# Optimization experiments

Measured on AMD Instinct MI355X. Metric: run time of the kernel, lower is better.

The kernel has to match this reference:

```python
import jax, jax.numpy as jnp
import numpy as np

B = 1
FRAMES = 16
P = 64            # patch_dim = image_size // patch_size = 256 // 4
C = 512           # query_dim == hidden_dim
T, HW, WW = 2, 8, 8   # window_size
NH = 8            # num_heads
HD = C // NH      # head_dim = 64
N = FRAMES * P * P


def setup_inputs() -> dict:
    key = jax.random.key(0)
    ks = jax.random.split(key, 5)
    x = jax.random.normal(ks[0], (B, N, C), dtype=jnp.float32)
    Wq = jax.random.normal(ks[1], (C, C), dtype=jnp.float32) * 0.02
    Wk = jax.random.normal(ks[2], (C, C), dtype=jnp.float32) * 0.02
    Wv = jax.random.normal(ks[3], (C, C), dtype=jnp.float32) * 0.02
    Wo = jax.random.normal(ks[4], (C, C), dtype=jnp.float32) * 0.02
    bo = jnp.zeros((C,), dtype=jnp.float32)
    return {"x": x, "Wq": Wq, "Wk": Wk, "Wv": Wv, "Wo": Wo, "bo": bo}


def reference(x, Wq, Wk, Wv, Wo, bo):
    nT, nH, nW = FRAMES // T, P // HW, P // WW
    L = T * HW * WW            # tokens per window = 128
    NWIN = nT * nH * nW        # 512 windows

    # window partition: [B,N,C] -> [B,nWin,L,C]
    xw = x.reshape(B, nT, T, nH, HW, nW, WW, C)
    xw = xw.transpose(0, 1, 3, 5, 2, 4, 6, 7).reshape(B, NWIN, L, C)

    # QKV projections (torch Linear: y = x @ W.T), split heads
    q = (xw @ Wq.T).reshape(B, NWIN, L, NH, HD)
    k = (xw @ Wk.T).reshape(B, NWIN, L, NH, HD)
    v = (xw @ Wv.T).reshape(B, NWIN, L, NH, HD)

    scale = 1.0 / jnp.sqrt(jnp.float32(HD))
    attn = jnp.einsum('bwqhd,bwkhd->bwhqk', q, k) * scale
    attn = jax.nn.softmax(attn, axis=-1)
    out = jnp.einsum('bwhqk,bwkhd->bwqhd', attn, v).reshape(B, NWIN, L, C)

    out = out @ Wo.T + bo      # output projection (dropout is identity at p=0/eval)

    # window merge: inverse of partition
    y = out.reshape(B, nT, nH, nW, T, HW, WW, C)
    y = y.transpose(0, 1, 4, 2, 5, 3, 6, 7).reshape(B, N, C)
    return y
```

## Files before the change

kernel.cpp:

```cpp
#include <hip/hip_runtime.h>


typedef __bf16 bf16x8 __attribute__((ext_vector_type(8)));
typedef float  f32x4  __attribute__((ext_vector_type(4)));

__device__ __forceinline__ unsigned short f2bf(float f) {
    unsigned int u = __float_as_uint(f);
    u += 0x7FFFu + ((u >> 16) & 1u);
    return (unsigned short)(u >> 16);
}
__device__ __forceinline__ unsigned int pack2(float lo, float hi) {
    return (unsigned int)f2bf(lo) | ((unsigned int)f2bf(hi) << 16);
}
__device__ __forceinline__ void glds16(const void* g, void* l) {
    __builtin_amdgcn_global_load_lds(
        (const __attribute__((address_space(1))) unsigned int*)g,
        (__attribute__((address_space(3))) unsigned int*)l, 16, 0, 0);
}

__global__ __launch_bounds__(256) void gather_cvt(const float* __restrict__ x,
                                                  unsigned short* __restrict__ xbf) {
    int tid = blockIdx.x * 256 + threadIdx.x;
    int r = tid >> 6;
    int c = (tid & 63) << 3;
    int w = r >> 7, l = r & 127;
    int wt = w >> 6, wy = (w >> 3) & 7, wx = w & 7;
    int lt = l >> 6, ly = (l >> 3) & 7, lx = l & 7;
    size_t n = (size_t)(wt * 2 + lt) * 4096 + (size_t)(wy * 8 + ly) * 64 + (wx * 8 + lx);
    const float4* s = (const float4*)(x + n * 512 + c);
    float4 a = s[0], b = s[1];
    uint4 o;
    o.x = pack2(a.x, a.y); o.y = pack2(a.z, a.w);
    o.z = pack2(b.x, b.y); o.w = pack2(b.z, b.w);
    *(uint4*)(xbf + (size_t)r * 512 + c) = o;
}

__global__ __launch_bounds__(256) void cvt_w4(const float* __restrict__ Wq,
                                              const float* __restrict__ Wk,
                                              const float* __restrict__ Wv,
                                              const float* __restrict__ Wo,
                                              unsigned short* __restrict__ d) {
    int b = blockIdx.x >> 7;
    int tid = (blockIdx.x & 127) * 256 + threadIdx.x;
    const float* s = (b == 0) ? Wq : (b == 1) ? Wk : (b == 2) ? Wv : Wo;
    const float4* sp = (const float4*)s + (size_t)tid * 2;
    float4 a = sp[0], bb = sp[1];
    uint4 o;
    o.x = pack2(a.x, a.y); o.y = pack2(a.z, a.w);
    o.z = pack2(bb.x, bb.y); o.w = pack2(bb.z, bb.w);
    ((uint4*)(d + (size_t)b * 262144))[tid] = o;
}


#define STAGE_A(tt, kh) do {                                                   \
    const unsigned short* g_ = Ap + (size_t)(tt) * 64 + (kh) * 32 + gOff;      \
    unsigned short* l_ = smem + ((((tt) & 1) * 2 + (kh)) * 8192);              \
    glds16(g_, l_ + j * 8);                                                    \
    glds16(g_ + 65536, l_ + 4096 + j * 8);                                     \
  } while (0)

#define STAGE_B(tt, kh) do {                                                   \
    const unsigned short* g_ = Bp + (size_t)(tt) * 64 + (kh) * 32 + gOff;      \
    unsigned short* l_ = smem + 32768 + ((((tt) & 1) * 2 + (kh)) * 8192);      \
    glds16(g_, l_ + j * 8);                                                    \
    glds16(g_ + 65536, l_ + 4096 + j * 8);                                     \
  } while (0)

#define PH_READA(d, ks, mh)                                                    \
    _Pragma("unroll") for (int i_ = 0; i_ < 4; ++i_)                           \
      af[i_] = *(const bf16x8*)(smem + ((d) * 2 + (ks)) * 8192 +               \
                                (arow + (mh) * 64 + i_ * 16) * 32 + ech);

#define PH_READB(d, ks)                                                        \
    _Pragma("unroll") for (int n_ = 0; n_ < 4; ++n_)                           \
      bfr[n_] = *(const bf16x8*)(smem + 32768 + ((d) * 2 + (ks)) * 8192 +      \
                                 (brow + n_ * 16) * 32 + ech);

#define PH_MFMA(mh)                                                            \
    __builtin_amdgcn_s_barrier();                                              \
    asm volatile("s_waitcnt lgkmcnt(0)" ::: "memory");                         \
    __builtin_amdgcn_sched_barrier(0);                                         \
    __builtin_amdgcn_s_setprio(1);                                             \
    _Pragma("unroll") for (int n_ = 0; n_ < 4; ++n_)                           \
      _Pragma("unroll") for (int i_ = 0; i_ < 4; ++i_)                         \
        acc[(mh) * 4 + i_][n_] = __builtin_amdgcn_mfma_f32_16x16x32_bf16(      \
            af[i_], bfr[n_], acc[(mh) * 4 + i_][n_], 0, 0, 0);                 \
    __builtin_amdgcn_s_setprio(0);                                             \
    __builtin_amdgcn_s_barrier();

#define GEMM8_MAIN_LOOP                                                        \
    STAGE_A(0, 0); STAGE_B(0, 0); STAGE_A(0, 1); STAGE_B(0, 1);                \
    STAGE_A(1, 0); STAGE_B(1, 0);                                              \
    asm volatile("s_waitcnt vmcnt(4)" ::: "memory");                           \
    __builtin_amdgcn_s_barrier();                                              \
    _Pragma("unroll 2")                                                        \
    for (int t = 0; t < 8; ++t) {                                              \
        const int d = t & 1;                                                   \
        PH_READA(d, 0, 0); PH_READB(d, 0);                                     \
        if (t < 7) STAGE_A(t + 1, 1);                                          \
        PH_MFMA(0);                                                            \
        PH_READA(d, 0, 1);                                                     \
        if (t < 7) {                                                           \
            STAGE_B(t + 1, 1);                                                 \
            asm volatile("s_waitcnt vmcnt(4)" ::: "memory");                   \
        }                                                                      \
        PH_MFMA(1);                                                            \
        PH_READA(d, 1, 0); PH_READB(d, 1);                                     \
        if (t < 6) STAGE_A(t + 2, 0);                                          \
        PH_MFMA(0);                                                            \
        PH_READA(d, 1, 1);                                                     \
        if (t < 6) {                                                           \
            STAGE_B(t + 2, 0);                                                 \
            asm volatile("s_waitcnt vmcnt(4)" ::: "memory");                   \
        } else if (t == 6) {                                                   \
            asm volatile("s_waitcnt vmcnt(0)" ::: "memory");                   \
        }                                                                      \
        PH_MFMA(1);                                                            \
    }

__global__ __launch_bounds__(512, 2) void qkv_gemm8(const unsigned short* __restrict__ xbf,
                                                    const unsigned short* __restrict__ wb,
                                                    unsigned short* __restrict__ Qb,
                                                    unsigned short* __restrict__ Kb,
                                                    unsigned short* __restrict__ Vb) {
    extern __shared__ unsigned short smem[];
    int id = blockIdx.x;
    int xcd = id & 7, rest = id >> 3;
    int rowblk = xcd * 32 + rest / 6;
    int colblk = rest % 6;

    const unsigned short* Ap = xbf + (size_t)rowblk * 131072;
    const unsigned short* Bp = wb + (size_t)colblk * 131072;

    int j = threadIdx.x;
    int lane = j & 63, wv = j >> 6;
    int wm = wv >> 2, wn = wv & 3;
    int quad = lane >> 4, lc = lane & 15;

    int r0 = j >> 2;
    int dcol = (((j & 3) ^ ((j >> 3) & 3)) << 3);
    const size_t gOff = (size_t)r0 * 512 + dcol;

    int arow = wm * 128 + lc;
    int brow = wn * 64 + lc;
    int ech = (quad ^ ((lc >> 1) & 3)) << 3;

    f32x4 acc[8][4] = {};
    bf16x8 af[4], bfr[4];

    GEMM8_MAIN_LOOP

    unsigned short* sc = smem + wv * 8192;
    int cb = colblk * 256 + wn * 64;
    int pj = cb >> 9;
    int h = (cb >> 6) & 7;
    int w2 = rowblk * 2 + wm;
    size_t ob = ((size_t)w2 * 8 + h) * 8192;

    if (pj == 2) {
        #pragma unroll
        for (int mi = 0; mi < 8; ++mi)
            #pragma unroll
            for (int n = 0; n < 4; ++n)
                #pragma unroll
                for (int rg = 0; rg < 4; ++rg) {
                    int l = mi * 16 + quad * 4 + rg;
                    int d2 = n * 16 + lc;
                    sc[d2 * 128 + (((l >> 3) ^ (d2 & 7)) << 3) + (l & 7)] =
                        f2bf(acc[mi][n][rg]);
                }
        asm volatile("s_waitcnt lgkmcnt(0)" ::: "memory");
        #pragma unroll
        for (int i = 0; i < 16; ++i) {
            int ci = i * 64 + lane;
            int d2 = ci >> 4, k = ci & 15;
            uint4 val = *(const uint4*)(sc + d2 * 128 + ((k ^ (d2 & 7)) << 3));
            *(uint4*)(Vb + ob + (size_t)ci * 8) = val;
        }
    } else {
        unsigned short* outp = pj ? Kb : Qb;
        float s = pj ? 1.0f : 0.125f;
        #pragma unroll
        for (int mi = 0; mi < 8; ++mi)
            #pragma unroll
            for (int n = 0; n < 4; ++n)
                #pragma unroll
                for (int rg = 0; rg < 4; ++rg) {
                    int l = mi * 16 + quad * 4 + rg;
                    int d2 = n * 16 + lc;
                    sc[l * 64 + (((d2 >> 3) ^ (l & 7)) << 3) + (d2 & 7)] =
                        f2bf(acc[mi][n][rg] * s);
                }
        asm volatile("s_waitcnt lgkmcnt(0)" ::: "memory");
        #pragma unroll
        for (int i = 0; i < 16; ++i) {
            int ci = i * 64 + lane;
            int l = ci >> 3, k = ci & 7;
            uint4 val = *(const uint4*)(sc + l * 64 + ((k ^ (l & 7)) << 3));
            *(uint4*)(outp + ob + (size_t)ci * 8) = val;
        }
    }
}

__global__ __launch_bounds__(256) void attn(const unsigned short* __restrict__ Qb,
                                            const unsigned short* __restrict__ Kb,
                                            const unsigned short* __restrict__ Vb,
                                            unsigned short* __restrict__ O) {
    int h = blockIdx.x, w = blockIdx.y;
    size_t base = ((size_t)w * 8 + h) * 8192;
    const unsigned short* q = Qb + base;
    const unsigned short* k = Kb + base;
    const unsigned short* v = Vb + base;

    __shared__ unsigned short smem[16384];
    unsigned short* sV = smem;
    unsigned short* sKP = smem + 8192;

    int t = threadIdx.x, lane = t & 63, wv = t >> 6;
    int quad = lane >> 4, lc = lane & 15;
    int sw = lc & 7;

    #pragma unroll
    for (int i = 0; i < 4; i++) {
        int s = t + i * 256;
        int r = s >> 3;
        int cq = ((s & 7) ^ (r & 7)) * 8;
        glds16(k + (size_t)r * 64 + cq, sKP + s * 8);
        int rv = s >> 4;
        int cv = (((s & 15) ^ (rv & 7))) * 8;
        glds16(v + (size_t)rv * 128 + cv, sV + s * 8);
    }

    bf16x8 aq[2][2];
    #pragma unroll
    for (int mi = 0; mi < 2; mi++)
        #pragma unroll
        for (int ks = 0; ks < 2; ks++)
            aq[mi][ks] = *(const bf16x8*)(q + (size_t)(wv * 32 + mi * 16 + lc) * 64 +
                                          ks * 32 + quad * 8);
    __syncthreads();

    f32x4 acc[2][8] = {};
    #pragma unroll
    for (int ks = 0; ks < 2; ks++) {
        int ch = ((quad + ks * 4) ^ sw) * 8;
        #pragma unroll
        for (int ni = 0; ni < 8; ni++) {
            bf16x8 bfr = *(const bf16x8*)(&sKP[(ni * 16 + lc) * 64 + ch]);
            #pragma unroll
            for (int mi = 0; mi < 2; mi++)
                acc[mi][ni] = __builtin_amdgcn_mfma_f32_16x16x32_bf16(aq[mi][ks], bfr, acc[mi][ni], 0, 0, 0);
        }
    }

    #pragma unroll
    for (int mi = 0; mi < 2; mi++)
        #pragma unroll
        for (int rg = 0; rg < 4; rg++) {
            float m = -1e30f;
            #pragma unroll
            for (int ni = 0; ni < 8; ni++) m = fmaxf(m, acc[mi][ni][rg]);
            #pragma unroll
            for (int off = 1; off < 16; off <<= 1) m = fmaxf(m, __shfl_xor(m, off, 64));
            float s = 0.f;
            #pragma unroll
            for (int ni = 0; ni < 8; ni++) {
                float e = __expf(acc[mi][ni][rg] - m);
                acc[mi][ni][rg] = e;
                s += e;
            }
            #pragma unroll
            for (int off = 1; off < 16; off <<= 1) s += __shfl_xor(s, off, 64);
            float inv = 1.0f / s;
            #pragma unroll
            for (int ni = 0; ni < 8; ni++) acc[mi][ni][rg] *= inv;
        }

    __syncthreads();

    f32x4 oc[2][4] = {};
    #pragma unroll
    for (int half = 0; half < 2; half++) {
        #pragma unroll
        for (int mi = 0; mi < 2; mi++)
            #pragma unroll
            for (int ni2 = 0; ni2 < 4; ni2++) {
                int ni = half * 4 + ni2;
                #pragma unroll
                for (int rg = 0; rg < 4; rg++) {
                    int r = wv * 32 + mi * 16 + quad * 4 + rg;
                    int c = ni2 * 16 + lc;
                    sKP[r * 64 + (((c >> 3) ^ (r & 7)) << 3) + (c & 7)] = f2bf(acc[mi][ni][rg]);
                }
            }
        asm volatile("s_waitcnt lgkmcnt(0)" ::: "memory");
        __builtin_amdgcn_sched_barrier(0);
        #pragma unroll
        for (int ks2 = 0; ks2 < 2; ks2++) {
            int chp = ((quad + ks2 * 4) ^ sw) * 8;
            int chv = (half * 8 + ((ks2 * 4 + quad) ^ sw)) * 8;
            bf16x8 af[2];
            #pragma unroll
            for (int mi = 0; mi < 2; mi++)
                af[mi] = *(const bf16x8*)(&sKP[(wv * 32 + mi * 16 + lc) * 64 + chp]);
            #pragma unroll
            for (int ni = 0; ni < 4; ni++) {
                bf16x8 bfr = *(const bf16x8*)(&sV[(ni * 16 + lc) * 128 + chv]);
                #pragma unroll
                for (int mi = 0; mi < 2; mi++)
                    oc[mi][ni] = __builtin_amdgcn_mfma_f32_16x16x32_bf16(af[mi], bfr, oc[mi][ni], 0, 0, 0);
            }
        }
    }

    #pragma unroll
    for (int mi = 0; mi < 2; mi++)
        #pragma unroll
        for (int ni = 0; ni < 4; ni++)
            #pragma unroll
            for (int rg = 0; rg < 4; rg++) {
                int l = wv * 32 + mi * 16 + quad * 4 + rg;
                int d = ni * 16 + lc;
                O[((size_t)w * 128 + l) * 512 + h * 64 + d] = f2bf(oc[mi][ni][rg]);
            }
}

__global__ __launch_bounds__(512, 2) void oproj_gemm8(const unsigned short* __restrict__ A,
                                                      const unsigned short* __restrict__ Bw,
                                                      const float* __restrict__ bo,
                                                      float* __restrict__ out) {
    extern __shared__ unsigned short smem[];
    int id = blockIdx.x;
    int xcd = id & 7, rest = id >> 3;
    int rowblk = xcd * 32 + (rest >> 1);
    int colblk = rest & 1;

    const unsigned short* Ap = A + (size_t)rowblk * 131072;
    const unsigned short* Bp = Bw + (size_t)colblk * 131072;

    int j = threadIdx.x;
    int lane = j & 63, wv = j >> 6;
    int wm = wv >> 2, wn = wv & 3;
    int quad = lane >> 4, lc = lane & 15;

    int r0 = j >> 2;
    int dcol = (((j & 3) ^ ((j >> 3) & 3)) << 3);
    const size_t gOff = (size_t)r0 * 512 + dcol;

    int arow = wm * 128 + lc;
    int brow = wn * 64 + lc;
    int ech = (quad ^ ((lc >> 1) & 3)) << 3;

    f32x4 acc[8][4] = {};
    bf16x8 af[4], bfr[4];

    GEMM8_MAIN_LOOP

    int cbase = colblk * 256 + wn * 64;
    float bias[4];
    #pragma unroll
    for (int ni = 0; ni < 4; ni++)
        bias[ni] = bo[cbase + ni * 16 + lc];

    #pragma unroll
    for (int mi = 0; mi < 8; ++mi)
        #pragma unroll
        for (int rg = 0; rg < 4; ++rg) {
            int r = rowblk * 256 + wm * 128 + mi * 16 + quad * 4 + rg;
            int w = r >> 7, l = r & 127;
            int wt = w >> 6, wy = (w >> 3) & 7, wx = w & 7;
            int lt = l >> 6, ly = (l >> 3) & 7, lx = l & 7;
            size_t n = (size_t)(wt * 2 + lt) * 4096 + (size_t)(wy * 8 + ly) * 64 + (wx * 8 + lx);
            #pragma unroll
            for (int ni = 0; ni < 4; ni++)
                out[n * 512 + cbase + ni * 16 + lc] = acc[mi][ni][rg] + bias[ni];
        }
}

extern "C" void kernel_launch(void* const* d_in, const int* in_sizes, int n_in,
                              void* d_out, int out_size, void* d_ws, size_t ws_size,
                              hipStream_t stream) {
    const float* x  = (const float*)d_in[0];
    const float* Wq = (const float*)d_in[1];
    const float* Wk = (const float*)d_in[2];
    const float* Wv = (const float*)d_in[3];
    const float* Wo = (const float*)d_in[4];
    const float* bo = (const float*)d_in[5];
    float* out = (float*)d_out;

    char* ws = (char*)d_ws;
    unsigned short* xbf = (unsigned short*)(ws);
    unsigned short* Qb  = (unsigned short*)(ws + 67108864);
    unsigned short* Kb  = (unsigned short*)(ws + 134217728);
    unsigned short* Vb  = (unsigned short*)(ws + 201326592);
    unsigned short* Wqb = (unsigned short*)(ws + 268435456);

    static bool attrset = false;
    if (!attrset) {
        (void)hipFuncSetAttribute(reinterpret_cast<const void*>(qkv_gemm8),
                                  hipFuncAttributeMaxDynamicSharedMemorySize, 131072);
        (void)hipFuncSetAttribute(reinterpret_cast<const void*>(oproj_gemm8),
                                  hipFuncAttributeMaxDynamicSharedMemorySize, 131072);
        attrset = true;
    }

    gather_cvt<<<16384, 256, 0, stream>>>(x, xbf);
    cvt_w4<<<512, 256, 0, stream>>>(Wq, Wk, Wv, Wo, Wqb);

    qkv_gemm8<<<1536, 512, 131072, stream>>>(xbf, Wqb, Qb, Kb, Vb);
    attn<<<dim3(8, 512), 256, 0, stream>>>(Qb, Kb, Vb, xbf);
    oproj_gemm8<<<512, 512, 131072, stream>>>(xbf, Wqb + 786432, bo, out);
}
```

Baseline: 474.4 us.

## Fuse QKV projection into per-window-head attention kernel

Replaces the separate QKV GEMM and attention kernels with one kernel where each block computes Q, K, V for one window and head directly from the bf16 input and weights, keeps them in shared memory, and runs softmax attention. This removes the round trip of writing and reading Q/K/V through global memory (three 64MB buffers) and one launch. The trade-off is that the x tile of each window is re-read once per head (8x) and the per-block GEMM is smaller (128x192x512), so operand reuse per load is lower than in the large-tile GEMM.

```diff
diff --git a/kernel.cpp b/kernel.cpp
--- a/kernel.cpp
+++ b/kernel.cpp
@@ -51,6 +51,185 @@
     ((uint4*)(d + (size_t)b * 262144))[tid] = o;
 }
 
+#define FSTAGE(tt) do {                                                        \
+    unsigned short* sb_ = smem + ((tt) & 1) * 20480;                           \
+    int k0_ = (tt) * 64;                                                       \
+    _Pragma("unroll") for (int i_ = 0; i_ < 4; ++i_) {                         \
+        int s_ = jj + i_ * 256, r_ = s_ >> 3;                                  \
+        int cq_ = ((s_ & 7) ^ (r_ & 7)) * 8;                                   \
+        glds16(Aw + (size_t)r_ * 512 + k0_ + cq_, sb_ + s_ * 8);               \
+    }                                                                          \
+    _Pragma("unroll") for (int p_ = 0; p_ < 3; ++p_)                           \
+      _Pragma("unroll") for (int i_ = 0; i_ < 2; ++i_) {                       \
+        int s_ = jj + i_ * 256, r_ = s_ >> 3;                                  \
+        int cq_ = ((s_ & 7) ^ (r_ & 7)) * 8;                                   \
+        glds16(Wp + (size_t)p_ * 262144 + (size_t)r_ * 512 + k0_ + cq_,        \
+               sb_ + 8192 + p_ * 4096 + s_ * 8);                               \
+    }                                                                          \
+  } while (0)
+
+__global__ __launch_bounds__(256, 2) void qkv_attn(const unsigned short* __restrict__ xbf,
+                                                   const unsigned short* __restrict__ wb,
+                                                   unsigned short* __restrict__ O) {
+    extern __shared__ unsigned short smem[];
+    int id = blockIdx.x;
+    int w = (id & 7) + ((id >> 6) << 3);
+    int h = (id >> 3) & 7;
+    const unsigned short* Aw = xbf + (size_t)w * 65536;
+    const unsigned short* Wp = wb + (size_t)h * 64 * 512;
+
+    int jj = threadIdx.x, lane = jj & 63, wv = jj >> 6;
+    int quad = lane >> 4, lc = lane & 15, sw = lc & 7;
+
+    f32x4 acc[3][2][4] = {};
+    FSTAGE(0);
+    for (int t = 0; t < 8; ++t) {
+        if (t < 7) {
+            FSTAGE(t + 1);
+            asm volatile("s_waitcnt vmcnt(10)" ::: "memory");
+        } else {
+            asm volatile("s_waitcnt vmcnt(0)" ::: "memory");
+        }
+        __builtin_amdgcn_s_barrier();
+        __builtin_amdgcn_sched_barrier(0);
+        const unsigned short* sb = smem + (t & 1) * 20480;
+        #pragma unroll
+        for (int ks = 0; ks < 2; ++ks) {
+            int ch = ((quad + ks * 4) ^ sw) * 8;
+            bf16x8 af[2];
+            #pragma unroll
+            for (int mi = 0; mi < 2; ++mi)
+                af[mi] = *(const bf16x8*)(sb + (wv * 32 + mi * 16 + lc) * 64 + ch);
+            #pragma unroll
+            for (int pj = 0; pj < 3; ++pj)
+                #pragma unroll
+                for (int ni = 0; ni < 4; ++ni) {
+                    bf16x8 bfr = *(const bf16x8*)(sb + 8192 + pj * 4096 +
+                                                  (ni * 16 + lc) * 64 + ch);
+                    #pragma unroll
+                    for (int mi = 0; mi < 2; ++mi)
+                        acc[pj][mi][ni] = __builtin_amdgcn_mfma_f32_16x16x32_bf16(
+                            af[mi], bfr, acc[pj][mi][ni], 0, 0, 0);
+                }
+        }
+        __builtin_amdgcn_s_barrier();
+        __builtin_amdgcn_sched_barrier(0);
+    }
+
+    unsigned short* sQ = smem;
+    unsigned short* sK = smem + 8192;
+    unsigned short* sV = smem + 16384;
+    unsigned short* sP = sK;
+    #pragma unroll
+    for (int mi = 0; mi < 2; ++mi)
+        #pragma unroll
+        for (int ni = 0; ni < 4; ++ni)
+            #pragma unroll
+            for (int rg = 0; rg < 4; ++rg) {
+                int l = wv * 32 + mi * 16 + quad * 4 + rg;
+                int d = ni * 16 + lc;
+                int qs = l * 64 + (((d >> 3) ^ (l & 7)) << 3) + (d & 7);
+                sQ[qs] = f2bf(acc[0][mi][ni][rg] * 0.125f);
+                sK[qs] = f2bf(acc[1][mi][ni][rg]);
+                sV[d * 128 + (((l >> 3) ^ (d & 7)) << 3) + (l & 7)] =
+                    f2bf(acc[2][mi][ni][rg]);
+            }
+    __syncthreads();
+
+    bf16x8 aq[2][2];
+    #pragma unroll
+    for (int mi = 0; mi < 2; ++mi)
+        #pragma unroll
+        for (int ks = 0; ks < 2; ++ks)
+            aq[mi][ks] = *(const bf16x8*)(sQ + (wv * 32 + mi * 16 + lc) * 64 +
+                                          (((quad + ks * 4) ^ sw) << 3));
+    f32x4 sacc[2][8] = {};
+    #pragma unroll
+    for (int ks = 0; ks < 2; ++ks) {
+        int ch = ((quad + ks * 4) ^ sw) * 8;
+        #pragma unroll
+        for (int ni = 0; ni < 8; ++ni) {
+            bf16x8 bfr = *(const bf16x8*)(&sK[(ni * 16 + lc) * 64 + ch]);
+            #pragma unroll
+            for (int mi = 0; mi < 2; ++mi)
+                sacc[mi][ni] = __builtin_amdgcn_mfma_f32_16x16x32_bf16(
+                    aq[mi][ks], bfr, sacc[mi][ni], 0, 0, 0);
+        }
+    }
+
+    #pragma unroll
+    for (int mi = 0; mi < 2; ++mi)
+        #pragma unroll
+        for (int rg = 0; rg < 4; ++rg) {
+            float m = -1e30f;
+            #pragma unroll
+            for (int ni = 0; ni < 8; ++ni) m = fmaxf(m, sacc[mi][ni][rg]);
+            #pragma unroll
+            for (int off = 1; off < 16; off <<= 1) m = fmaxf(m, __shfl_xor(m, off, 64));
+            float s = 0.f;
+            #pragma unroll
+            for (int ni = 0; ni < 8; ++ni) {
+                float e = __expf(sacc[mi][ni][rg] - m);
+                sacc[mi][ni][rg] = e;
+                s += e;
+            }
+            #pragma unroll
+            for (int off = 1; off < 16; off <<= 1) s += __shfl_xor(s, off, 64);
+            float inv = 1.0f / s;
+            #pragma unroll
+            for (int ni = 0; ni < 8; ni++) sacc[mi][ni][rg] *= inv;
+        }
+
+    __syncthreads();
+
+    f32x4 oc[2][4] = {};
+    #pragma unroll
+    for (int half = 0; half < 2; ++half) {
+        #pragma unroll
+        for (int mi = 0; mi < 2; ++mi)
+            #pragma unroll
+            for (int ni2 = 0; ni2 < 4; ++ni2) {
+                int ni = half * 4 + ni2;
+                #pragma unroll
+                for (int rg = 0; rg < 4; ++rg) {
+                    int r = wv * 32 + mi * 16 + quad * 4 + rg;
+                    int c = ni2 * 16 + lc;
+                    sP[r * 64 + (((c >> 3) ^ (r & 7)) << 3) + (c & 7)] =
+                        f2bf(sacc[mi][ni][rg]);
+                }
+            }
+        asm volatile("s_waitcnt lgkmcnt(0)" ::: "memory");
+        __builtin_amdgcn_sched_barrier(0);
+        #pragma unroll
+        for (int ks2 = 0; ks2 < 2; ++ks2) {
+            int chp = ((quad + ks2 * 4) ^ sw) * 8;
+            int chv = (half * 8 + ((ks2 * 4 + quad) ^ sw)) * 8;
+            bf16x8 af[2];
+            #pragma unroll
+            for (int mi = 0; mi < 2; ++mi)
+                af[mi] = *(const bf16x8*)(&sP[(wv * 32 + mi * 16 + lc) * 64 + chp]);
+            #pragma unroll
+            for (int ni = 0; ni < 4; ++ni) {
+                bf16x8 bfr = *(const bf16x8*)(&sV[(ni * 16 + lc) * 128 + chv]);
+                #pragma unroll
+                for (int mi = 0; mi < 2; ++mi)
+                    oc[mi][ni] = __builtin_amdgcn_mfma_f32_16x16x32_bf16(
+                        af[mi], bfr, oc[mi][ni], 0, 0, 0);
+            }
+        }
+    }
+
+    #pragma unroll
+    for (int mi = 0; mi < 2; ++mi)
+        #pragma unroll
+        for (int ni = 0; ni < 4; ++ni)
+            #pragma unroll
+            for (int rg = 0; rg < 4; ++rg) {
+                int l = wv * 32 + mi * 16 + quad * 4 + rg;
+                int d = ni * 16 + lc;
+                O[((size_t)w * 128 + l) * 512 + h * 64 + d] = f2bf(oc[mi][ni][rg]);
+            }
+}
 
 #define STAGE_A(tt, kh) do {                                                   \
     const unsigned short* g_ = Ap + (size_t)(tt) * 64 + (kh) * 32 + gOff;      \
@@ -118,213 +297,6 @@
         PH_MFMA(1);                                                            \
     }
 
-__global__ __launch_bounds__(512, 2) void qkv_gemm8(const unsigned short* __restrict__ xbf,
-                                                    const unsigned short* __restrict__ wb,
-                                                    unsigned short* __restrict__ Qb,
-                                                    unsigned short* __restrict__ Kb,
-                                                    unsigned short* __restrict__ Vb) {
-    extern __shared__ unsigned short smem[];
-    int id = blockIdx.x;
-    int xcd = id & 7, rest = id >> 3;
-    int rowblk = xcd * 32 + rest / 6;
-    int colblk = rest % 6;
-
-    const unsigned short* Ap = xbf + (size_t)rowblk * 131072;
-    const unsigned short* Bp = wb + (size_t)colblk * 131072;
-
-    int j = threadIdx.x;
-    int lane = j & 63, wv = j >> 6;
-    int wm = wv >> 2, wn = wv & 3;
-    int quad = lane >> 4, lc = lane & 15;
-
-    int r0 = j >> 2;
-    int dcol = (((j & 3) ^ ((j >> 3) & 3)) << 3);
-    const size_t gOff = (size_t)r0 * 512 + dcol;
-
-    int arow = wm * 128 + lc;
-    int brow = wn * 64 + lc;
-    int ech = (quad ^ ((lc >> 1) & 3)) << 3;
-
-    f32x4 acc[8][4] = {};
-    bf16x8 af[4], bfr[4];
-
-    GEMM8_MAIN_LOOP
-
-    unsigned short* sc = smem + wv * 8192;
-    int cb = colblk * 256 + wn * 64;
-    int pj = cb >> 9;
-    int h = (cb >> 6) & 7;
-    int w2 = rowblk * 2 + wm;
-    size_t ob = ((size_t)w2 * 8 + h) * 8192;
-
-    if (pj == 2) {
-        #pragma unroll
-        for (int mi = 0; mi < 8; ++mi)
-            #pragma unroll
-            for (int n = 0; n < 4; ++n)
-                #pragma unroll
-                for (int rg = 0; rg < 4; ++rg) {
-                    int l = mi * 16 + quad * 4 + rg;
-                    int d2 = n * 16 + lc;
-                    sc[d2 * 128 + (((l >> 3) ^ (d2 & 7)) << 3) + (l & 7)] =
-                        f2bf(acc[mi][n][rg]);
-                }
-        asm volatile("s_waitcnt lgkmcnt(0)" ::: "memory");
-        #pragma unroll
-        for (int i = 0; i < 16; ++i) {
-            int ci = i * 64 + lane;
-            int d2 = ci >> 4, k = ci & 15;
-            uint4 val = *(const uint4*)(sc + d2 * 128 + ((k ^ (d2 & 7)) << 3));
-            *(uint4*)(Vb + ob + (size_t)ci * 8) = val;
-        }
-    } else {
-        unsigned short* outp = pj ? Kb : Qb;
-        float s = pj ? 1.0f : 0.125f;
-        #pragma unroll
-        for (int mi = 0; mi < 8; ++mi)
-            #pragma unroll
-            for (int n = 0; n < 4; ++n)
-                #pragma unroll
-                for (int rg = 0; rg < 4; ++rg) {
-                    int l = mi * 16 + quad * 4 + rg;
-                    int d2 = n * 16 + lc;
-                    sc[l * 64 + (((d2 >> 3) ^ (l & 7)) << 3) + (d2 & 7)] =
-                        f2bf(acc[mi][n][rg] * s);
-                }
-        asm volatile("s_waitcnt lgkmcnt(0)" ::: "memory");
-        #pragma unroll
-        for (int i = 0; i < 16; ++i) {
-            int ci = i * 64 + lane;
-            int l = ci >> 3, k = ci & 7;
-            uint4 val = *(const uint4*)(sc + l * 64 + ((k ^ (l & 7)) << 3));
-            *(uint4*)(outp + ob + (size_t)ci * 8) = val;
-        }
-    }
-}
-
-__global__ __launch_bounds__(256) void attn(const unsigned short* __restrict__ Qb,
-                                            const unsigned short* __restrict__ Kb,
-                                            const unsigned short* __restrict__ Vb,
-                                            unsigned short* __restrict__ O) {
-    int h = blockIdx.x, w = blockIdx.y;
-    size_t base = ((size_t)w * 8 + h) * 8192;
-    const unsigned short* q = Qb + base;
-    const unsigned short* k = Kb + base;
-    const unsigned short* v = Vb + base;
-
-    __shared__ unsigned short smem[16384];
-    unsigned short* sV = smem;
-    unsigned short* sKP = smem + 8192;
-
-    int t = threadIdx.x, lane = t & 63, wv = t >> 6;
-    int quad = lane >> 4, lc = lane & 15;
-    int sw = lc & 7;
-
-    #pragma unroll
-    for (int i = 0; i < 4; i++) {
-        int s = t + i * 256;
-        int r = s >> 3;
-        int cq = ((s & 7) ^ (r & 7)) * 8;
-        glds16(k + (size_t)r * 64 + cq, sKP + s * 8);
-        int rv = s >> 4;
-        int cv = (((s & 15) ^ (rv & 7))) * 8;
-        glds16(v + (size_t)rv * 128 + cv, sV + s * 8);
-    }
-
-    bf16x8 aq[2][2];
-    #pragma unroll
-    for (int mi = 0; mi < 2; mi++)
-        #pragma unroll
-        for (int ks = 0; ks < 2; ks++)
-            aq[mi][ks] = *(const bf16x8*)(q + (size_t)(wv * 32 + mi * 16 + lc) * 64 +
-                                          ks * 32 + quad * 8);
-    __syncthreads();
-
-    f32x4 acc[2][8] = {};
-    #pragma unroll
-    for (int ks = 0; ks < 2; ks++) {
-        int ch = ((quad + ks * 4) ^ sw) * 8;
-        #pragma unroll
-        for (int ni = 0; ni < 8; ni++) {
-            bf16x8 bfr = *(const bf16x8*)(&sKP[(ni * 16 + lc) * 64 + ch]);
-            #pragma unroll
-            for (int mi = 0; mi < 2; mi++)
-                acc[mi][ni] = __builtin_amdgcn_mfma_f32_16x16x32_bf16(aq[mi][ks], bfr, acc[mi][ni], 0, 0, 0);
-        }
-    }
-
-    #pragma unroll
-    for (int mi = 0; mi < 2; mi++)
-        #pragma unroll
-        for (int rg = 0; rg < 4; rg++) {
-            float m = -1e30f;
-            #pragma unroll
-            for (int ni = 0; ni < 8; ni++) m = fmaxf(m, acc[mi][ni][rg]);
-            #pragma unroll
-            for (int off = 1; off < 16; off <<= 1) m = fmaxf(m, __shfl_xor(m, off, 64));
-            float s = 0.f;
-            #pragma unroll
-            for (int ni = 0; ni < 8; ni++) {
-                float e = __expf(acc[mi][ni][rg] - m);
-                acc[mi][ni][rg] = e;
-                s += e;
-            }
-            #pragma unroll
-            for (int off = 1; off < 16; off <<= 1) s += __shfl_xor(s, off, 64);
-            float inv = 1.0f / s;
-            #pragma unroll
-            for (int ni = 0; ni < 8; ni++) acc[mi][ni][rg] *= inv;
-        }
-
-    __syncthreads();
-
-    f32x4 oc[2][4] = {};
-    #pragma unroll
-    for (int half = 0; half < 2; half++) {
-        #pragma unroll
-        for (int mi = 0; mi < 2; mi++)
-            #pragma unroll
-            for (int ni2 = 0; ni2 < 4; ni2++) {
-                int ni = half * 4 + ni2;
-                #pragma unroll
-                for (int rg = 0; rg < 4; rg++) {
-                    int r = wv * 32 + mi * 16 + quad * 4 + rg;
-                    int c = ni2 * 16 + lc;
-                    sKP[r * 64 + (((c >> 3) ^ (r & 7)) << 3) + (c & 7)] = f2bf(acc[mi][ni][rg]);
-                }
-            }
-        asm volatile("s_waitcnt lgkmcnt(0)" ::: "memory");
-        __builtin_amdgcn_sched_barrier(0);
-        #pragma unroll
-        for (int ks2 = 0; ks2 < 2; ks2++) {
-            int chp = ((quad + ks2 * 4) ^ sw) * 8;
-            int chv = (half * 8 + ((ks2 * 4 + quad) ^ sw)) * 8;
-            bf16x8 af[2];
-            #pragma unroll
-            for (int mi = 0; mi < 2; mi++)
-                af[mi] = *(const bf16x8*)(&sKP[(wv * 32 + mi * 16 + lc) * 64 + chp]);
-            #pragma unroll
-            for (int ni = 0; ni < 4; ni++) {
-                bf16x8 bfr = *(const bf16x8*)(&sV[(ni * 16 + lc) * 128 + chv]);
-                #pragma unroll
-                for (int mi = 0; mi < 2; mi++)
-                    oc[mi][ni] = __builtin_amdgcn_mfma_f32_16x16x32_bf16(af[mi], bfr, oc[mi][ni], 0, 0, 0);
-            }
-        }
-    }
-
-    #pragma unroll
-    for (int mi = 0; mi < 2; mi++)
-        #pragma unroll
-        for (int ni = 0; ni < 4; ni++)
-            #pragma unroll
-            for (int rg = 0; rg < 4; rg++) {
-                int l = wv * 32 + mi * 16 + quad * 4 + rg;
-                int d = ni * 16 + lc;
-                O[((size_t)w * 128 + l) * 512 + h * 64 + d] = f2bf(oc[mi][ni][rg]);
-            }
-}
-
 __global__ __launch_bounds__(512, 2) void oproj_gemm8(const unsigned short* __restrict__ A,
                                                       const unsigned short* __restrict__ Bw,
                                                       const float* __restrict__ bo,
@@ -390,15 +362,13 @@
 
     char* ws = (char*)d_ws;
     unsigned short* xbf = (unsigned short*)(ws);
-    unsigned short* Qb  = (unsigned short*)(ws + 67108864);
-    unsigned short* Kb  = (unsigned short*)(ws + 134217728);
-    unsigned short* Vb  = (unsigned short*)(ws + 201326592);
+    unsigned short* Ob  = (unsigned short*)(ws + 67108864);
     unsigned short* Wqb = (unsigned short*)(ws + 268435456);
 
     static bool attrset = false;
     if (!attrset) {
-        (void)hipFuncSetAttribute(reinterpret_cast<const void*>(qkv_gemm8),
-                                  hipFuncAttributeMaxDynamicSharedMemorySize, 131072);
+        (void)hipFuncSetAttribute(reinterpret_cast<const void*>(qkv_attn),
+                                  hipFuncAttributeMaxDynamicSharedMemorySize, 81920);
         (void)hipFuncSetAttribute(reinterpret_cast<const void*>(oproj_gemm8),
                                   hipFuncAttributeMaxDynamicSharedMemorySize, 131072);
         attrset = true;
@@ -407,7 +377,6 @@
     gather_cvt<<<16384, 256, 0, stream>>>(x, xbf);
     cvt_w4<<<512, 256, 0, stream>>>(Wq, Wk, Wv, Wo, Wqb);
 
-    qkv_gemm8<<<1536, 512, 131072, stream>>>(xbf, Wqb, Qb, Kb, Vb);
-    attn<<<dim3(8, 512), 256, 0, stream>>>(Qb, Kb, Vb, xbf);
-    oproj_gemm8<<<512, 512, 131072, stream>>>(xbf, Wqb + 786432, bo, out);
-}
+    qkv_attn<<<4096, 256, 81920, stream>>>(xbf, Wqb, Ob);
+    oproj_gemm8<<<512, 512, 131072, stream>>>(Ob, Wqb + 786432, bo, out);
+}
```

Measured after the change: 418.7 us. 1.13x faster.
